# Performance work log

Measured on AMD Instinct MI355X. Metric: run time of the kernel, lower is better.

## Reference

```python
import jax, jax.numpy as jnp
import numpy as np

N_NODES = 50000


def gcn_conv(x, edge_index, W, b, n_nodes):
    # PyG GCNConv: add self-loops, symmetric normalization, linear, scatter-add.
    src, dst = edge_index[0], edge_index[1]
    loops = jnp.arange(n_nodes, dtype=src.dtype)
    src = jnp.concatenate([src, loops])
    dst = jnp.concatenate([dst, loops])
    # linear transform first (PyG order), reduces scatter width when out < in
    h = x @ W  # [N, out]
    deg = jax.ops.segment_sum(jnp.ones_like(dst, dtype=h.dtype), dst, num_segments=n_nodes)
    dinv = jnp.where(deg > 0, jax.lax.rsqrt(deg), 0.0)
    norm = dinv[src] * dinv[dst]  # [E+N]
    msgs = h[src] * norm[:, None]  # gather + scale, [E+N, out]
    out = jax.ops.segment_sum(msgs, dst, num_segments=n_nodes)  # scatter-add
    return out + b


def setup_inputs() -> dict:
    key = jax.random.key(0)
    k1, k2, k3, k4 = jax.random.split(key, 4)
    in_c, hid_c, out_c = 256, 128, 64
    n_edges = 800000
    features = jax.random.normal(k1, (N_NODES, in_c), dtype=jnp.float32)
    edge_index = jax.random.randint(k2, (2, n_edges), 0, N_NODES, dtype=jnp.int64)
    W1 = jax.random.normal(k3, (in_c, hid_c), dtype=jnp.float32) * (1.0 / np.sqrt(in_c))
    b1 = jnp.zeros((hid_c,), dtype=jnp.float32)
    W2 = jax.random.normal(k4, (hid_c, out_c), dtype=jnp.float32) * (1.0 / np.sqrt(hid_c))
    b2 = jnp.zeros((out_c,), dtype=jnp.float32)
    return {"features": features, "edge_index": edge_index, "W1": W1, "b1": b1, "W2": W2, "b2": b2}


def reference(features, edge_index, W1, b1, W2, b2):
    n = features.shape[0]
    x = gcn_conv(features, edge_index, W1, b1, n)
    x = jax.nn.relu(x)
    # dropout p=0.5 is identity at inference
    x = gcn_conv(x, edge_index, W2, b2, n)
    return x
```

## Files before the change

### kernel.cpp

```cpp
#include <hip/hip_runtime.h>

#define THREADS 256
#define SEG 64

typedef _Float16 f16;
typedef f16   f16x8 __attribute__((ext_vector_type(8)));
typedef float f32x4 __attribute__((ext_vector_type(4)));
typedef float fvec4 __attribute__((ext_vector_type(4)));

__global__ void k_zero(unsigned* __restrict__ cnt, int n4){
  int i = blockIdx.x*blockDim.x + threadIdx.x;
  if(i < n4) ((int4*)cnt)[i] = make_int4(0,0,0,0);
}

__global__ void k_build(const int* __restrict__ ei, unsigned* __restrict__ cnt,
                        unsigned short* __restrict__ ssrc, int E, int M){
  const int grp = blockIdx.x & 7;
  const int nb  = blockIdx.x >> 3;
  const int lo  = grp * (M >> 3);
  const int hi  = (grp == 7) ? M : lo + (M >> 3);
  int e = nb*THREADS + threadIdx.x;
  if(e < E){
    int d = __builtin_nontemporal_load(ei + E + e);
    if(d >= lo && d < hi){
      int s = __builtin_nontemporal_load(ei + e);
      unsigned p = atomicAdd(&cnt[d], 1u);
      if(p < SEG) ssrc[(size_t)d*SEG + p] = (unsigned short)s;
    }
  }
}

template<int K, int N>
__global__ void k_gemm1(const float* __restrict__ A, const float* __restrict__ W,
                        const unsigned* __restrict__ cnt, f16* __restrict__ Hh, int M){
  constexpr int BM = 64, BK = 32, BN = N;
  constexpr int AST = 40;
  constexpr int NM = 4, NN = 2;
  constexpr int SKN = BK*BN/THREADS;
  __shared__ f16 Ah[BM*AST], Bh[BN*AST];

  const int tid  = threadIdx.x;
  const int row0 = blockIdx.x*BM;
  const int wc = tid>>6, l = tid&63;
  const int lr = l&15, lk = l>>4;

  const int sar = tid>>2, sak = (tid&3)*8;
  const long long garow = min(row0+sar, M-1);
  const int sc = tid & (BN-1), sk0 = (tid>>7)*SKN;

  f32x4 acc[NM][NN] = {};

  for(int k0 = 0; k0 < K; k0 += BK){
    float avals[8];
    #pragma unroll
    for(int q=0;q<2;q++){
      fvec4 v = __builtin_nontemporal_load((const fvec4*)(A + garow*K + k0 + sak + q*4));
      avals[q*4+0]=v.x; avals[q*4+1]=v.y; avals[q*4+2]=v.z; avals[q*4+3]=v.w;
    }
    float bvals[SKN];
    #pragma unroll
    for(int i=0;i<SKN;i++) bvals[i] = W[(size_t)(k0+sk0+i)*N + sc];

    __syncthreads();

    {
      f16x8 hv;
      #pragma unroll
      for(int j=0;j<8;j++) hv[j] = (f16)avals[j];
      *(f16x8*)&Ah[sar*AST + sak] = hv;
    }
    #pragma unroll
    for(int s=0;s<SKN/8;s++){
      f16x8 hv;
      #pragma unroll
      for(int j=0;j<8;j++) hv[j] = (f16)bvals[s*8+j];
      *(f16x8*)&Bh[sc*AST + sk0 + s*8] = hv;
    }
    __syncthreads();

    f16x8 af[NM], bf[NN];
    #pragma unroll
    for(int m=0;m<NM;m++){
      int r = m*16 + lr;
      af[m] = *(const f16x8*)&Ah[r*AST + lk*8];
    }
    #pragma unroll
    for(int n=0;n<NN;n++){
      int c = wc*32 + n*16 + lr;
      bf[n] = *(const f16x8*)&Bh[c*AST + lk*8];
    }
    #pragma unroll
    for(int m=0;m<NM;m++)
      #pragma unroll
      for(int n=0;n<NN;n++)
        acc[m][n] = __builtin_amdgcn_mfma_f32_16x16x32_f16(af[m], bf[n], acc[m][n], 0,0,0);
  }

  #pragma unroll
  for(int m=0;m<NM;m++){
    int grb = row0 + m*16 + lk*4;
    #pragma unroll
    for(int reg=0;reg<4;reg++){
      int gr = grb + reg;
      if(gr < M){
        float dv = rsqrtf((float)(cnt[gr] + 1u));
        #pragma unroll
        for(int n=0;n<NN;n++){
          int gc = wc*32 + n*16 + lr;
          Hh[(size_t)gr*N + gc] = (f16)(acc[m][n][reg] * dv);
        }
      }
    }
  }
}

template<int K, int N>
__global__ void k_gemm_mfma_f16a(const f16* __restrict__ A, const float* __restrict__ W,
                                 const unsigned* __restrict__ cnt, f16* __restrict__ Hh, int M){
  constexpr int BM = 64, BK = 32, BN = N;
  constexpr int AST = 40;
  constexpr int NM = 4;
  constexpr int SKN = BK*BN/THREADS;
  __shared__ f16 Ah[BM*AST], Bh[BN*AST];

  const int tid  = threadIdx.x;
  const int row0 = blockIdx.x*BM;
  const int wc = tid>>6, l = tid&63;
  const int lr = l&15, lk = l>>4;

  const int sar = tid>>2, sak = (tid&3)*8;
  const long long garow = min(row0+sar, M-1);
  const int sc = tid & (BN-1), sk0 = (tid>>6)*SKN;

  f32x4 acc[NM] = {};

  for(int k0 = 0; k0 < K; k0 += BK){
    f16x8 av = *(const f16x8*)(A + garow*K + k0 + sak);
    float bvals[SKN];
    #pragma unroll
    for(int i=0;i<SKN;i++) bvals[i] = W[(size_t)(k0+sk0+i)*N + sc];

    __syncthreads();

    *(f16x8*)&Ah[sar*AST + sak] = av;
    {
      f16x8 hv;
      #pragma unroll
      for(int j=0;j<8;j++) hv[j] = (f16)bvals[j];
      *(f16x8*)&Bh[sc*AST + sk0] = hv;
    }
    __syncthreads();

    f16x8 af[NM], bf;
    #pragma unroll
    for(int m=0;m<NM;m++){
      int r = m*16 + lr;
      af[m] = *(const f16x8*)&Ah[r*AST + lk*8];
    }
    {
      int c = wc*16 + lr;
      bf = *(const f16x8*)&Bh[c*AST + lk*8];
    }
    #pragma unroll
    for(int m=0;m<NM;m++)
      acc[m] = __builtin_amdgcn_mfma_f32_16x16x32_f16(af[m], bf, acc[m], 0,0,0);
  }

  #pragma unroll
  for(int m=0;m<NM;m++){
    int grb = row0 + m*16 + lk*4;
    #pragma unroll
    for(int reg=0;reg<4;reg++){
      int gr = grb + reg;
      if(gr < M){
        float dv = rsqrtf((float)(cnt[gr] + 1u));
        int gc = wc*16 + lr;
        Hh[(size_t)gr*N + gc] = (f16)(acc[m][reg] * dv);
      }
    }
  }
}

__global__ void k_gather_l1(const unsigned* __restrict__ cnt,
                            const unsigned short* __restrict__ ssrc,
                            const f16* __restrict__ g,
                            const float* __restrict__ bias, f16* __restrict__ outh, int M){
  const int w = (blockIdx.x*blockDim.x + threadIdx.x) >> 6;
  const int l = threadIdx.x & 63;
  if(w >= M) return;
  const int q = l>>4, c = l&15;
  const f16x8* g8 = (const f16x8*)g;
  float acc[8] = {0.f,0.f,0.f,0.f,0.f,0.f,0.f,0.f};
  const int ne = min((int)cnt[w], SEG);
  int it = ne >> 2;
  int i = w*SEG + q;
  while(it >= 2){
    int s0 = (int)ssrc[i], s1 = (int)ssrc[i+4];
    f16x8 v0 = g8[(size_t)s0*16 + c];
    f16x8 v1 = g8[(size_t)s1*16 + c];
    #pragma unroll
    for(int j=0;j<8;j++) acc[j] += (float)v0[j] + (float)v1[j];
    i += 8; it -= 2;
  }
  if(it){
    int s = (int)ssrc[i];
    f16x8 v = g8[(size_t)s*16 + c];
    #pragma unroll
    for(int j=0;j<8;j++) acc[j] += (float)v[j];
    i += 4;
  }
  if(q < (ne & 3)){
    int s = (int)ssrc[i];
    f16x8 v = g8[(size_t)s*16 + c];
    #pragma unroll
    for(int j=0;j<8;j++) acc[j] += (float)v[j];
  }
  if(q == 0){
    f16x8 v = g8[(size_t)w*16 + c];
    #pragma unroll
    for(int j=0;j<8;j++) acc[j] += (float)v[j];
  }
  #pragma unroll
  for(int j=0;j<8;j++){
    acc[j] += __shfl_xor(acc[j], 16);
    acc[j] += __shfl_xor(acc[j], 32);
  }
  if(q == 0){
    const float dw = rsqrtf((float)(cnt[w] + 1u));
    float4 b0 = ((const float4*)bias)[c*2];
    float4 b1 = ((const float4*)bias)[c*2+1];
    f16x8 o;
    o[0] = (f16)fmaxf(fmaf(acc[0], dw, b0.x), 0.f);
    o[1] = (f16)fmaxf(fmaf(acc[1], dw, b0.y), 0.f);
    o[2] = (f16)fmaxf(fmaf(acc[2], dw, b0.z), 0.f);
    o[3] = (f16)fmaxf(fmaf(acc[3], dw, b0.w), 0.f);
    o[4] = (f16)fmaxf(fmaf(acc[4], dw, b1.x), 0.f);
    o[5] = (f16)fmaxf(fmaf(acc[5], dw, b1.y), 0.f);
    o[6] = (f16)fmaxf(fmaf(acc[6], dw, b1.z), 0.f);
    o[7] = (f16)fmaxf(fmaf(acc[7], dw, b1.w), 0.f);
    ((f16x8*)outh)[(size_t)w*16 + c] = o;
  }
}

__global__ void k_gather_l2(const unsigned* __restrict__ cnt,
                            const unsigned short* __restrict__ ssrc,
                            const f16* __restrict__ g,
                            const float* __restrict__ bias, float* __restrict__ out, int M){
  const int w = (blockIdx.x*blockDim.x + threadIdx.x) >> 6;
  const int l = threadIdx.x & 63;
  if(w >= M) return;
  const int grp = l>>3, c = l&7;
  const f16x8* g8 = (const f16x8*)g;
  float acc[8] = {0.f,0.f,0.f,0.f,0.f,0.f,0.f,0.f};
  const int ne = min((int)cnt[w], SEG);
  int it = ne >> 3;
  int i = w*SEG + grp;
  while(it >= 2){
    int s0 = (int)ssrc[i], s1 = (int)ssrc[i+8];
    f16x8 v0 = g8[(size_t)s0*8 + c];
    f16x8 v1 = g8[(size_t)s1*8 + c];
    #pragma unroll
    for(int j=0;j<8;j++) acc[j] += (float)v0[j] + (float)v1[j];
    i += 16; it -= 2;
  }
  if(it){
    int s = (int)ssrc[i];
    f16x8 v = g8[(size_t)s*8 + c];
    #pragma unroll
    for(int j=0;j<8;j++) acc[j] += (float)v[j];
    i += 8;
  }
  if(grp < (ne & 7)){
    int s = (int)ssrc[i];
    f16x8 v = g8[(size_t)s*8 + c];
    #pragma unroll
    for(int j=0;j<8;j++) acc[j] += (float)v[j];
  }
  if(grp == 0){
    f16x8 v = g8[(size_t)w*8 + c];
    #pragma unroll
    for(int j=0;j<8;j++) acc[j] += (float)v[j];
  }
  #pragma unroll
  for(int j=0;j<8;j++){
    acc[j] += __shfl_xor(acc[j], 8);
    acc[j] += __shfl_xor(acc[j], 16);
    acc[j] += __shfl_xor(acc[j], 32);
  }
  if(grp == 0){
    const float dw = rsqrtf((float)(cnt[w] + 1u));
    float4 b0 = ((const float4*)bias)[c*2];
    float4 b1 = ((const float4*)bias)[c*2+1];
    float4 o0, o1;
    o0.x = fmaf(acc[0], dw, b0.x);
    o0.y = fmaf(acc[1], dw, b0.y);
    o0.z = fmaf(acc[2], dw, b0.z);
    o0.w = fmaf(acc[3], dw, b0.w);
    o1.x = fmaf(acc[4], dw, b1.x);
    o1.y = fmaf(acc[5], dw, b1.y);
    o1.z = fmaf(acc[6], dw, b1.z);
    o1.w = fmaf(acc[7], dw, b1.w);
    ((float4*)out)[(size_t)w*16 + c*2]     = o0;
    ((float4*)out)[(size_t)w*16 + c*2 + 1] = o1;
  }
}

extern "C" void kernel_launch(void* const* d_in, const int* in_sizes, int n_in,
                              void* d_out, int out_size, void* d_ws, size_t ws_size,
                              hipStream_t stream){
  const float* feat = (const float*)d_in[0];
  const int*   ei   = (const int*)d_in[1];
  const float* W1   = (const float*)d_in[2];
  const float* b1   = (const float*)d_in[3];
  const float* W2   = (const float*)d_in[4];
  const float* b2   = (const float*)d_in[5];
  float* out = (float*)d_out;

  const int M = in_sizes[0] / 256;
  const int E = in_sizes[1] / 2;

  float* ws = (float*)d_ws;
  unsigned*       cnt  = (unsigned*)ws;
  unsigned short* ssrc = (unsigned short*)(ws + 51200);
  f16*            h1h  = (f16*)(ws + 1651200);
  f16*            o1h  = (f16*)(ws + 4851200);
  f16*            h2h  = h1h;

  const int nbE = (E + THREADS-1)/THREADS;
  const int gemmBlocks = (M + 63)/64;
  const int n4 = (M + 3)/4;

  k_zero<<<(n4 + THREADS-1)/THREADS, THREADS, 0, stream>>>(cnt, n4);
  k_build<<<nbE*8, THREADS, 0, stream>>>(ei, cnt, ssrc, E, M);

  k_gemm1<256,128><<<gemmBlocks, THREADS, 0, stream>>>(feat, W1, cnt, h1h, M);
  k_gather_l1<<<(M*64 + THREADS-1)/THREADS, THREADS, 0, stream>>>(cnt, ssrc, h1h, b1, o1h, M);

  k_gemm_mfma_f16a<128,64><<<gemmBlocks, THREADS, 0, stream>>>(o1h, W2, cnt, h2h, M);
  k_gather_l2<<<(M*64 + THREADS-1)/THREADS, THREADS, 0, stream>>>(cnt, ssrc, h2h, b2, out, M);
}
```

Baseline: 142.1 us.

## Use persistent XCC-aware work-stealing blocks for CSR build with vector loads

```diff
diff --git a/kernel.cpp b/kernel.cpp
--- a/kernel.cpp
+++ b/kernel.cpp
@@ -2,30 +2,61 @@
 
 #define THREADS 256
 #define SEG 64
+#define CH  1024
 
 typedef _Float16 f16;
 typedef f16   f16x8 __attribute__((ext_vector_type(8)));
 typedef float f32x4 __attribute__((ext_vector_type(4)));
 typedef float fvec4 __attribute__((ext_vector_type(4)));
+typedef int   ivec4 __attribute__((ext_vector_type(4)));
 
 __global__ void k_zero(unsigned* __restrict__ cnt, int n4){
   int i = blockIdx.x*blockDim.x + threadIdx.x;
   if(i < n4) ((int4*)cnt)[i] = make_int4(0,0,0,0);
 }
 
+__device__ __forceinline__ int xcc_id(){
+  int x;
+  asm volatile("s_getreg_b32 %0, hwreg(HW_REG_XCC_ID)" : "=s"(x));
+  return x & 7;
+}
+
 __global__ void k_build(const int* __restrict__ ei, unsigned* __restrict__ cnt,
-                        unsigned short* __restrict__ ssrc, int E, int M){
-  const int grp = blockIdx.x & 7;
-  const int nb  = blockIdx.x >> 3;
-  const int lo  = grp * (M >> 3);
-  const int hi  = (grp == 7) ? M : lo + (M >> 3);
-  int e = nb*THREADS + threadIdx.x;
-  if(e < E){
-    int d = __builtin_nontemporal_load(ei + E + e);
-    if(d >= lo && d < hi){
-      int s = __builtin_nontemporal_load(ei + e);
-      unsigned p = atomicAdd(&cnt[d], 1u);
-      if(p < SEG) ssrc[(size_t)d*SEG + p] = (unsigned short)s;
+                        unsigned short* __restrict__ ssrc, int* __restrict__ tickets,
+                        int E, int M, int nChunks){
+  __shared__ int sj;
+  const int grp0 = xcc_id();
+  for(int gi=0; gi<8; ++gi){
+    const int grp = (grp0 + gi) & 7;
+    const int lo  = grp * (M >> 3);
+    const int hi  = (grp == 7) ? M : lo + (M >> 3);
+    while(true){
+      if(threadIdx.x == 0) sj = atomicAdd(&tickets[grp], 1);
+      __syncthreads();
+      const int j = sj;
+      __syncthreads();
+      if(j >= nChunks) break;
+      int e0 = j*CH + (int)threadIdx.x*4;
+      if(e0 < E){
+        ivec4 d4;
+        if(e0 + 3 < E){
+          d4 = __builtin_nontemporal_load((const ivec4*)(ei + E + e0));
+        } else {
+          d4.x = ei[E+e0];
+          d4.y = (e0+1<E)? ei[E+e0+1] : -1;
+          d4.z = (e0+2<E)? ei[E+e0+2] : -1;
+          d4.w = (e0+3<E)? ei[E+e0+3] : -1;
+        }
+        #pragma unroll
+        for(int t=0;t<4;t++){
+          int d = (t==0)? d4.x : (t==1)? d4.y : (t==2)? d4.z : d4.w;
+          if(d >= lo && d < hi){
+            int s = __builtin_nontemporal_load(ei + e0 + t);
+            unsigned p = atomicAdd(&cnt[d], 1u);
+            if(p < SEG) ssrc[(size_t)d*SEG + p] = (unsigned short)s;
+          }
+        }
+      }
     }
   }
 }
@@ -321,17 +352,18 @@
 
   float* ws = (float*)d_ws;
   unsigned*       cnt  = (unsigned*)ws;
+  int*            tick = (int*)(ws + 50176);
   unsigned short* ssrc = (unsigned short*)(ws + 51200);
   f16*            h1h  = (f16*)(ws + 1651200);
   f16*            o1h  = (f16*)(ws + 4851200);
   f16*            h2h  = h1h;
 
-  const int nbE = (E + THREADS-1)/THREADS;
   const int gemmBlocks = (M + 63)/64;
-  const int n4 = (M + 3)/4;
+  const int nChunks = (E + CH-1)/CH;
+  const int n4 = (50176 + 8 + 3)/4;
 
   k_zero<<<(n4 + THREADS-1)/THREADS, THREADS, 0, stream>>>(cnt, n4);
-  k_build<<<nbE*8, THREADS, 0, stream>>>(ei, cnt, ssrc, E, M);
+  k_build<<<1024, THREADS, 0, stream>>>(ei, cnt, ssrc, tick, E, M, nChunks);
 
   k_gemm1<256,128><<<gemmBlocks, THREADS, 0, stream>>>(feat, W1, cnt, h1h, M);
   k_gather_l1<<<(M*64 + THREADS-1)/THREADS, THREADS, 0, stream>>>(cnt, ssrc, h1h, b1, o1h, M);
```

Measured after the change: 279.8 us. +96.9%, slower.
